# Kernel optimization log

Measured on AMD Instinct MI355X. Metric: run time of the kernel, lower is better.

Reference implementation:

```python
import jax, jax.numpy as jnp
import numpy as np

B, C, H, W = 64, 128, 56, 56
ALPHA = 0.001


def _build_inhi_mat(out_channels):
    # Circulant 0/1 band: row i has ones at columns (i-r//2 ... i+r//2) mod C,
    # exactly matching the torch double loop with modular wrap-around.
    r = out_channels // 8 + 1  # inhiRange
    i = np.arange(out_channels)[:, None]
    d = np.arange(-(r // 2), r // 2 + 1)[None, :]
    cols = (i + d) % out_channels  # [C, r]
    m = np.zeros((out_channels, out_channels), dtype=np.float32)
    m[np.repeat(i, d.shape[1], axis=1), cols] = 1.0
    return m


def setup_inputs() -> dict:
    key = jax.random.key(0)
    x = jax.random.normal(key, (B, C, H, W), dtype=jnp.float32)
    inhiMat = jnp.asarray(_build_inhi_mat(C))  # [C, C] constant buffer
    return {"x": x, "inhiMat": inhiMat}


def reference(x, inhiMat):
    b, c, h, w = x.shape
    inhiRange = c // 8 + 1
    # y = detach(x)^2 -> banded cross-channel sum (bmm with broadcast [C,C] mat)
    y = jax.lax.stop_gradient(x) ** 2
    y = y.reshape(b, c, h * w)
    y = jnp.einsum('ij,bjs->bis', inhiMat, y)  # same math as bmm with tiled inhi
    y = y.reshape(b, c, h, w)
    denom = (y * ALPHA / inhiRange + 1.0) ** 0.75
    return x / denom
```

## Files before the change

kernel.cpp:

```cpp
#include <hip/hip_runtime.h>


#define HW4 784
#define CSTR HW4
#define BSTR4 (128 * HW4)
#define NCOL4 (64 * HW4)
#define TILE 16
#define NBLK (NCOL4 / TILE)

typedef __attribute__((address_space(3))) unsigned int lds_u32;
typedef __attribute__((address_space(1))) const unsigned int glb_u32;

__device__ __forceinline__ float pow_m075(float t) {
    return __builtin_amdgcn_exp2f(-0.75f * __builtin_amdgcn_logf(t));
}

__global__ __launch_bounds__(256, 5) void lrn_kernel(const float4* __restrict__ x,
                                                     float4* __restrict__ out) {
    const float kAlphaOverR = 0.001f / 17.0f;

    __shared__ float4 lds[128 * TILE];

    const int tid  = threadIdx.x;
    const int lane = tid & 63;
    const int wave = tid >> 6;

    {
        const int cl    = lane & 15;
        const int pp    = lane >> 4;
        const int col4g = blockIdx.x * TILE + cl;
        const int b     = col4g / HW4;
        const int hw4   = col4g - b * HW4;
        const float4* src0 = x + (size_t)b * BSTR4 + hw4 + (size_t)pp * CSTR;
#pragma unroll
        for (int j = 0; j < 8; ++j) {
            const int q = wave * 8 + j;
            __builtin_amdgcn_global_load_lds((glb_u32*)(src0 + (size_t)q * (4 * CSTR)),
                                             (lds_u32*)&lds[q * 64], 16, 0, 0);
        }
    }
    asm volatile("s_waitcnt vmcnt(0)" ::: "memory");
    __syncthreads();

    const int c   = tid & 15;
    const int ch0 = (tid >> 4) * 8;

    const int col4g = blockIdx.x * TILE + c;
    const int b     = col4g / HW4;
    const int hw4   = col4g - b * HW4;
    float4* obase   = out + (size_t)b * BSTR4 + hw4;

    float sx = 0.f, sy = 0.f, sz = 0.f, sw = 0.f;
#pragma unroll
    for (int j = -8; j <= 8; ++j) {
        const float4 v = lds[((ch0 + j) & 127) * TILE + c];
        sx = fmaf(v.x, v.x, sx);
        sy = fmaf(v.y, v.y, sy);
        sz = fmaf(v.z, v.z, sz);
        sw = fmaf(v.w, v.w, sw);
    }

#pragma unroll
    for (int i = 0; i < 8; ++i) {
        const int ch = ch0 + i;
        const float4 xc = lds[ch * TILE + c];
        float4 o;
        o.x = xc.x * pow_m075(fmaf(sx, kAlphaOverR, 1.0f));
        o.y = xc.y * pow_m075(fmaf(sy, kAlphaOverR, 1.0f));
        o.z = xc.z * pow_m075(fmaf(sz, kAlphaOverR, 1.0f));
        o.w = xc.w * pow_m075(fmaf(sw, kAlphaOverR, 1.0f));
        obase[(size_t)ch * CSTR] = o;

        if (i < 7) {
            const float4 a = lds[((ch + 9) & 127) * TILE + c];
            const float4 d = lds[((ch - 8) & 127) * TILE + c];
            sx += a.x * a.x - d.x * d.x;
            sy += a.y * a.y - d.y * d.y;
            sz += a.z * a.z - d.z * d.z;
            sw += a.w * a.w - d.w * d.w;
        }
    }
}

extern "C" void kernel_launch(void* const* d_in, const int* in_sizes, int n_in,
                              void* d_out, int out_size, void* d_ws, size_t ws_size,
                              hipStream_t stream) {
    const float4* x = (const float4*)d_in[0];
    float4* out = (float4*)d_out;

    dim3 grid(NBLK);
    lrn_kernel<<<grid, 256, 0, stream>>>(x, out);
}
```

Before: 183.1 us.

## Give each wave its own haloed channel band to drop block barrier

Each wave now loads its own 32-channel band plus an 8-channel halo on each side (48 planes) into a private LDS region. Because a wave only reads data it loaded itself, the block-wide __syncthreads is removed and waves can proceed independently. The cost is 1.5x global reads for halo channels and LDS growing from 32KB to 48KB per block. The launch-bounds occupancy hint of 5 is also dropped.

```diff
diff --git a/kernel.cpp b/kernel.cpp
--- a/kernel.cpp
+++ b/kernel.cpp
@@ -6,6 +6,8 @@
 #define BSTR4 (128 * HW4)
 #define NCOL4 (64 * HW4)
 #define TILE 16
+#define SEGC 32
+#define PLANES 48
 #define NBLK (NCOL4 / TILE)
 
 typedef __attribute__((address_space(3))) unsigned int lds_u32;
@@ -15,45 +17,39 @@
     return __builtin_amdgcn_exp2f(-0.75f * __builtin_amdgcn_logf(t));
 }
 
-__global__ __launch_bounds__(256, 5) void lrn_kernel(const float4* __restrict__ x,
-                                                     float4* __restrict__ out) {
+__global__ __launch_bounds__(256) void lrn_kernel(const float4* __restrict__ x,
+                                                  float4* __restrict__ out) {
     const float kAlphaOverR = 0.001f / 17.0f;
 
-    __shared__ float4 lds[128 * TILE];
+    __shared__ float4 lds[4 * PLANES * TILE];
 
     const int tid  = threadIdx.x;
     const int lane = tid & 63;
     const int wave = tid >> 6;
+    const int band = wave * SEGC;
 
-    {
-        const int cl    = lane & 15;
-        const int pp    = lane >> 4;
-        const int col4g = blockIdx.x * TILE + cl;
-        const int b     = col4g / HW4;
-        const int hw4   = col4g - b * HW4;
-        const float4* src0 = x + (size_t)b * BSTR4 + hw4 + (size_t)pp * CSTR;
+    float4* buf = &lds[wave * (PLANES * TILE)];
+
+    const int cl    = lane & 15;
+    const int g     = lane >> 4;
+    const int col4g = blockIdx.x * TILE + cl;
+    const int b     = col4g / HW4;
+    const int hw4   = col4g - b * HW4;
+    const float4* xbase = x + (size_t)b * BSTR4 + hw4;
+    float4*       obase = out + (size_t)b * BSTR4 + hw4;
+
 #pragma unroll
-        for (int j = 0; j < 8; ++j) {
-            const int q = wave * 8 + j;
-            __builtin_amdgcn_global_load_lds((glb_u32*)(src0 + (size_t)q * (4 * CSTR)),
-                                             (lds_u32*)&lds[q * 64], 16, 0, 0);
-        }
+    for (int q = 0; q < 12; ++q) {
+        const int ch = (band - 8 + 4 * q + g + 128) & 127;
+        __builtin_amdgcn_global_load_lds((glb_u32*)(xbase + (size_t)ch * CSTR),
+                                         (lds_u32*)&buf[q * 64], 16, 0, 0);
     }
     asm volatile("s_waitcnt vmcnt(0)" ::: "memory");
-    __syncthreads();
-
-    const int c   = tid & 15;
-    const int ch0 = (tid >> 4) * 8;
-
-    const int col4g = blockIdx.x * TILE + c;
-    const int b     = col4g / HW4;
-    const int hw4   = col4g - b * HW4;
-    float4* obase   = out + (size_t)b * BSTR4 + hw4;
 
     float sx = 0.f, sy = 0.f, sz = 0.f, sw = 0.f;
 #pragma unroll
-    for (int j = -8; j <= 8; ++j) {
-        const float4 v = lds[((ch0 + j) & 127) * TILE + c];
+    for (int j = 0; j < 17; ++j) {
+        const float4 v = buf[(g * 8 + j) * TILE + cl];
         sx = fmaf(v.x, v.x, sx);
         sy = fmaf(v.y, v.y, sy);
         sz = fmaf(v.z, v.z, sz);
@@ -62,18 +58,18 @@
 
 #pragma unroll
     for (int i = 0; i < 8; ++i) {
-        const int ch = ch0 + i;
-        const float4 xc = lds[ch * TILE + c];
+        const int j = g * 8 + 8 + i;
+        const float4 xc = buf[j * TILE + cl];
         float4 o;
         o.x = xc.x * pow_m075(fmaf(sx, kAlphaOverR, 1.0f));
         o.y = xc.y * pow_m075(fmaf(sy, kAlphaOverR, 1.0f));
         o.z = xc.z * pow_m075(fmaf(sz, kAlphaOverR, 1.0f));
         o.w = xc.w * pow_m075(fmaf(sw, kAlphaOverR, 1.0f));
-        obase[(size_t)ch * CSTR] = o;
+        obase[(size_t)(band + g * 8 + i) * CSTR] = o;
 
         if (i < 7) {
-            const float4 a = lds[((ch + 9) & 127) * TILE + c];
-            const float4 d = lds[((ch - 8) & 127) * TILE + c];
+            const float4 a = buf[(j + 9) * TILE + cl];
+            const float4 d = buf[(j - 8) * TILE + cl];
             sx += a.x * a.x - d.x * d.x;
             sy += a.y * a.y - d.y * d.y;
             sz += a.z * a.z - d.z * d.z;
```

After: 182.3 us. No clear change (-0.4%).
